# Kernel tuning notes

Hardware: AMD Instinct MI355X
Metric: run time of the kernel (lower is better)

The kernel has to match this reference:

```python
import jax, jax.numpy as jnp
import numpy as np
import math

FS = 44100.0
HOP = 256
N_BANDS = 24
KS_BUF = 768  # > max delay 44100/60 = 735 samples


def _lpc1(x, a):
    # order-1 all-pole (sample_wise_lpc with order 1, per-batch constant coeff):
    # y[n] = x[n] - a*y[n-1];  x: [B,N], a: [B]
    def step(yp, xt):
        y = xt - a * yp
        return y, y
    _, ys = jax.lax.scan(step, jnp.zeros_like(a), x.T)
    return ys.T


def _diff_ks(f0_frames, exc, l_b):
    # differentiable Karplus-Strong: fractional-delay loop + 2-tap damping filter.
    # f0_frames: [B,F] Hz, exc: [B,N], l_b: [B,F,2] (loop_coeff, loop_mix logits)
    B, N = exc.shape
    g = 0.999 * jax.nn.sigmoid(l_b[..., 0])   # loop gain in (0, 0.999)
    s = jax.nn.sigmoid(l_b[..., 1])           # loop-filter mix
    up = lambda p: jnp.repeat(p, HOP, axis=1)[:, :N]
    g_s, s_s = up(g), up(s)
    f0_s = up(jnp.clip(f0_frames, 60.0, None))
    D = jnp.clip(FS / f0_s, 2.0, 735.0)        # delay in samples
    Di = jnp.floor(D).astype(jnp.int32)
    fr = (D - Di).astype(exc.dtype)
    L = KS_BUF

    def step(carry, xs):
        buf, n = carry                         # buf: [B,L] circular delay line
        x_t, Di_t, fr_t, g_t, s_t = xs         # each [B]
        i1 = jnp.mod(n - Di_t, L)
        i2 = jnp.mod(n - Di_t - 1, L)
        i3 = jnp.mod(n - Di_t - 2, L)
        take = lambda i: jnp.take_along_axis(buf, i[:, None], axis=1)[:, 0]
        b1, b2, b3 = take(i1), take(i2), take(i3)
        z = (1.0 - fr_t) * b1 + fr_t * b2      # fractional-delay read y[n-D]
        z1 = (1.0 - fr_t) * b2 + fr_t * b3     # y[n-D-1]
        y = x_t + g_t * ((1.0 - s_t) * z + s_t * z1)
        buf = buf.at[:, jnp.mod(n, L)].set(y)
        return (buf, n + 1), y

    xs = (exc.T, Di.T, fr.T, g_s.T, s_s.T)
    init = (jnp.zeros((B, L), exc.dtype), jnp.int32(0))
    _, ys = jax.lax.scan(step, init, xs)
    return ys.T


def _body(x, body_gains):
    # bank of 24 two-pole resonators, log-spaced 80..8000 Hz, Q=10
    fc = jnp.geomspace(80.0, 8000.0, N_BANDS).astype(x.dtype)
    w = 2.0 * jnp.pi * fc / FS
    r = jnp.exp(-jnp.pi * fc / (10.0 * FS))
    a1 = -2.0 * r * jnp.cos(w)
    a2 = r * r
    b0 = 1.0 - r
    B = x.shape[0]

    def step(carry, xt):
        y1, y2 = carry                          # [B,24] each
        y = b0 * xt[:, None] - a1 * y1 - a2 * y2
        return (y, y1), jnp.sum(y * body_gains, axis=-1)

    init = (jnp.zeros((B, N_BANDS), x.dtype), jnp.zeros((B, N_BANDS), x.dtype))
    _, out = jax.lax.scan(step, init, x.T)
    return out.T


def _forward(excitation, pitch, w1, b1, w2, b2, excitation_gain, body_gains):
    B, _, N = excitation.shape
    h = jax.nn.relu(pitch @ w1.T + b1)
    mlp_out = h @ w2.T + b2                     # [B,3]
    loop_coeff = jnp.clip(mlp_out[:, 0], -2.0, 2.5)
    loop_mix = jnp.clip(mlp_out[:, 1], -2.5, 0.0)
    frames = N // HOP
    l_b = jnp.broadcast_to(jnp.stack([loop_coeff, loop_mix], -1)[:, None, :], (B, frames, 2))
    f0_frames = jnp.broadcast_to(pitch, (B, frames))
    exc_sq = (excitation * excitation_gain)[:, 0, :]
    f0_hz = jnp.clip(pitch[:, 0], 60.0, None)
    mult = jnp.clip(2.0 + 6.0 * (f0_hz - 60.0) / 600.0, 2.0, 8.0)
    cutoff = jnp.minimum(2.0 * jnp.pi * f0_hz * mult / FS, jnp.pi * 0.9)
    alpha = 1.0 - jnp.exp(-cutoff)
    exc_f = _lpc1(exc_sq * alpha[:, None], alpha - 1.0)   # pre-KS one-pole LP
    string = _diff_ks(f0_frames, exc_f, l_b)
    loop_post = jnp.clip(mlp_out[:, 2], -4.0, 4.0)
    cutoff_post = jnp.minimum(jnp.pi * jax.nn.sigmoid(loop_post), jnp.pi * 0.99)
    alpha_p = 1.0 - jnp.exp(-cutoff_post)
    string = _lpc1(string * alpha_p[:, None], alpha_p - 1.0)  # post one-pole LP
    out = _body(string, body_gains)
    return out[:, None, :], loop_coeff.mean(), loop_mix.mean(), loop_post.mean()


def setup_inputs():
    key = jax.random.key(0)
    k = jax.random.split(key, 6)
    B, N = 8, 32768
    excitation = jax.random.normal(k[0], (B, 1, N), dtype=jnp.float32)
    pitch = 60.0 + 600.0 * jax.random.uniform(k[1], (B, 1), dtype=jnp.float32)
    bnd1 = 0.1 * math.sqrt(6.0 / (1 + 16))   # xavier_uniform, gain 0.1
    bnd2 = 0.1 * math.sqrt(6.0 / (16 + 3))
    w1 = jax.random.uniform(k[2], (16, 1), jnp.float32, -bnd1, bnd1)
    b1 = jnp.zeros((16,), jnp.float32)
    w2 = jax.random.uniform(k[3], (3, 16), jnp.float32, -bnd2, bnd2)
    b2 = jnp.array([0.9, 0.0, 0.0], jnp.float32)
    excitation_gain = jnp.array(0.25, jnp.float32)
    body_gains = 0.006 * jnp.ones((1, N_BANDS), jnp.float32)
    return {"excitation": excitation, "pitch": pitch, "w1": w1, "b1": b1,
            "w2": w2, "b2": b2, "excitation_gain": excitation_gain,
            "body_gains": body_gains}


def reference(excitation, pitch, w1, b1, w2, b2, excitation_gain, body_gains):
    return _forward(excitation, pitch, w1, b1, w2, b2, excitation_gain, body_gains)
```

## Files before the change

kernel.cpp:

```cpp
#include <hip/hip_runtime.h>
#include <math.h>

#define NSAMP 32768
#define FS_F 44100.0f
#define PI_F 3.14159265358979323846f
#define T1 1024
#define FLAG_MAGIC 0x5A5A5A5A

#define XALL_FLOATS 33792
#define PROG_OFF 33792
#define TABS_OFF 33808
#define SMEM_FLOATS 40720

struct BParams {
  float alpha, alpha_p;
  float fr, g, s;
  int Di;
  float lc, lm, lp;
};

__device__ inline float sigmoidf_(float x) { return 1.0f / (1.0f + expf(-x)); }

__device__ inline BParams compute_params(int b, const float* __restrict__ pitch,
                                         const float* __restrict__ w1,
                                         const float* __restrict__ b1,
                                         const float* __restrict__ w2,
                                         const float* __restrict__ b2) {
  BParams P;
  float p = pitch[b];
  float h[16];
#pragma unroll
  for (int i = 0; i < 16; ++i) {
    float v = fmaf(p, w1[i], b1[i]);
    h[i] = v > 0.0f ? v : 0.0f;
  }
  float m[3];
#pragma unroll
  for (int j = 0; j < 3; ++j) {
    float acc = b2[j];
#pragma unroll
    for (int i = 0; i < 16; ++i) acc = fmaf(h[i], w2[j * 16 + i], acc);
    m[j] = acc;
  }
  P.lc = fminf(fmaxf(m[0], -2.0f), 2.5f);
  P.lm = fminf(fmaxf(m[1], -2.5f), 0.0f);
  P.lp = fminf(fmaxf(m[2], -4.0f), 4.0f);
  P.g = 0.999f * sigmoidf_(P.lc);
  P.s = sigmoidf_(P.lm);
  float f0 = fmaxf(p, 60.0f);
  float D = fminf(fmaxf(FS_F / f0, 2.0f), 735.0f);
  int Di = (int)floorf(D);
  P.fr = D - (float)Di;
  P.Di = Di;
  float mult = fminf(fmaxf(2.0f + 6.0f * (f0 - 60.0f) / 600.0f, 2.0f), 8.0f);
  float cutoff = fminf(2.0f * PI_F * f0 * mult / FS_F, PI_F * 0.9f);
  P.alpha = 1.0f - expf(-cutoff);
  float cpost = fminf(PI_F * sigmoidf_(P.lp), PI_F * 0.99f);
  P.alpha_p = 1.0f - expf(-cpost);
  return P;
}

__device__ inline float rlv(float v, int l) {
  return __int_as_float(__builtin_amdgcn_readlane(__float_as_int(v), l));
}
__device__ inline float shr1(float v, float bnd) {
  return __int_as_float(__builtin_amdgcn_update_dpp(
      __float_as_int(bnd), __float_as_int(v), 0x138 , 0xf, 0xf,
      false));
}
__device__ inline float ror1(float v) {
  return __int_as_float(__builtin_amdgcn_update_dpp(
      __float_as_int(v), __float_as_int(v), 0x13C , 0xf, 0xf,
      false));
}

__device__ inline void band_coef(int k, float& a1, float& a2, float& b0) {
  float fc = 80.0f * exp2f((float)k * (6.64385618977472436f / 23.0f));
  float w = 2.0f * PI_F * fc / FS_F;
  float r = expf(-PI_F * fc / (10.0f * FS_F));
  a1 = -2.0f * r * cosf(w);
  a2 = r * r;
  b0 = 1.0f - r;
}

__device__ inline void gen_tables(float* __restrict__ tabs, int W) {
  if (W >= 120) return;
  const int j = W / 5, sub = W % 5;
  float A1, A2, B0;
  band_coef(j, A1, A2, B0);
  if (sub == 0) *(float4*)&tabs[j * 4] = make_float4(A1, A2, B0, 0.f);
  float Q00 = -A1, Q01 = -A2, Q10 = 1.f, Q11 = 0.f;
#pragma unroll
  for (int sq = 0; sq < 2; ++sq) {
    float n00 = fmaf(Q00, Q00, Q01 * Q10);
    float n01 = fmaf(Q00, Q01, Q01 * Q11);
    float n10 = fmaf(Q10, Q00, Q11 * Q10);
    float n11 = fmaf(Q10, Q01, Q11 * Q11);
    Q00 = n00; Q01 = n01; Q10 = n10; Q11 = n11;
  }
  float K00 = Q00, K01 = Q01, K10 = Q10, K11 = Q11;
#pragma unroll
  for (int sq = 0; sq < 2; ++sq) {
    float n00 = fmaf(Q00, Q00, Q01 * Q10);
    float n01 = fmaf(Q00, Q01, Q01 * Q11);
    float n10 = fmaf(Q10, Q00, Q11 * Q10);
    float n11 = fmaf(Q10, Q01, Q11 * Q11);
    Q00 = n00; Q01 = n01; Q10 = n10; Q11 = n11;
  }
  float L00[7], L01[7], L10[7], L11[7];
  L00[0] = fmaf(Q00, K00, Q01 * K10);
  L01[0] = fmaf(Q00, K01, Q01 * K11);
  L10[0] = fmaf(Q10, K00, Q11 * K10);
  L11[0] = fmaf(Q10, K01, Q11 * K11);
#pragma unroll
  for (int k = 0; k < 6; ++k) {
    float s00 = fmaf(L00[k], L00[k], L01[k] * L10[k]);
    float s01 = fmaf(L00[k], L01[k], L01[k] * L11[k]);
    float s10 = fmaf(L10[k], L00[k], L11[k] * L10[k]);
    float s11 = fmaf(L10[k], L01[k], L11[k] * L11[k]);
    L00[k + 1] = s00; L01[k + 1] = s01; L10[k + 1] = s10; L11[k + 1] = s11;
  }
  if (sub == 0) {
#pragma unroll
    for (int k = 0; k < 6; ++k)
      *(float4*)&tabs[96 + (k * 24 + j) * 4] =
          make_float4(L00[k], L01[k], L10[k], L11[k]);
    *(float4*)&tabs[672 + j * 4] = make_float4(L00[6], L01[6], L10[6], L11[6]);
  }
  int l0 = sub * 13, l1 = l0 + 13;
  if (l1 > 64) l1 = 64;
  for (int l = l0; l < l1; ++l) {
    float R00 = 1.f, R01 = 0.f, R10 = 0.f, R11 = 1.f;
#pragma unroll
    for (int bit = 0; bit < 6; ++bit) {
      if ((l >> bit) & 1) {
        float n00 = fmaf(L00[bit], R00, L01[bit] * R10);
        float n01 = fmaf(L00[bit], R01, L01[bit] * R11);
        float n10 = fmaf(L10[bit], R00, L11[bit] * R10);
        float n11 = fmaf(L10[bit], R01, L11[bit] * R11);
        R00 = n00; R01 = n01; R10 = n10; R11 = n11;
      }
    }
    *(float4*)&tabs[768 + (j * 64 + l) * 4] = make_float4(R00, R01, R10, R11);
  }
}

__device__ inline void w1_load(const float* __restrict__ xg, int s1, int seg,
                               int lane, float4* pf) {
  const int base = s1 + (seg << 11) + (lane << 5);
#pragma unroll
  for (int i = 0; i < 8; ++i) {
    const int g = base + 4 * i;
    float4 v = make_float4(0.f, 0.f, 0.f, 0.f);
    if (g >= 0 && g + 3 < NSAMP) v = *(const float4*)&xg[g];
    pf[i] = v;
  }
}

#define KS_STEP(STORES)                                                       \
  do {                                                                        \
    float b2v[KNUM], b3v[KNUM];                                               \
    b2v[0] = shr1(yp[0], p1);                                                 \
    _Pragma("unroll") for (int k = 1; k < KNUM; ++k)                          \
        b2v[k] = shr1(yp[k], ror1(yp[k - 1]));                                \
    b3v[0] = shr1(b2v[0], p2);                                                \
    _Pragma("unroll") for (int k = 1; k < KNUM; ++k)                          \
        b3v[k] = shr1(b2v[k], ror1(b2v[k - 1]));                              \
    float p1n = rlv(yp[KNUM - 1], lq1);                                       \
    float p2n = rlv(b2v[KNUM - 1], lq1);                                      \
    _Pragma("unroll") for (int k = 0; k < KNUM; ++k)                          \
        yp[k] =                                                               \
            fmaf(c0w, yp[k], fmaf(c2w, b3v[k], fmaf(c1w, b2v[k], xC[k])));    \
    p1 = p1n;                                                                 \
    p2 = p2n;                                                                 \
    if (STORES) {                                                             \
      _Pragma("unroll") for (int k = 0; k < KNUM; ++k) {                      \
        int i = lane + (k << 6);                                              \
        int n = s1 + rel + i;                                                 \
        bool okl = (k < KNUM - 1) || (lane <= lq1);                           \
        if (okl && n >= n0 && n < end) yg[n] = yp[k];                         \
      }                                                                       \
    }                                                                         \
    int r2 = rel + 2 * C;                                                     \
    if (r2 < span) {                                                          \
      const float* xp = &xall[r2 + lane];                                     \
      _Pragma("unroll") for (int k = 0; k < KNUM; ++k) {                      \
        xC[k] = xN[k];                                                        \
        xN[k] = xp[k << 6];                                                   \
      }                                                                       \
    } else {                                                                  \
      _Pragma("unroll") for (int k = 0; k < KNUM; ++k) xC[k] = xN[k];         \
    }                                                                         \
    rel += C;                                                                 \
  } while (0)

template <int KNUM>
__device__ void ks_wave0(float* __restrict__ yg, const float* xall,
                         int* __restrict__ prog, int lane, int C, float c0w,
                         float c1w, float c2w, int s1, int n0, int end,
                         int span, int NSG) {
  const int lq1 = (C - 1) - (KNUM - 1) * 64;
  const int W = n0 - s1;
  float yp[KNUM], xC[KNUM], xN[KNUM];
  float p1 = 0.f, p2 = 0.f;
  int rel = 0;
#pragma unroll
  for (int k = 0; k < KNUM; ++k) { yp[k] = 0.f; xC[k] = 0.f; xN[k] = 0.f; }
  for (int s = 0; s < NSG; ++s) {
    int need = s + 3;
    if (need > NSG) need = NSG;
    while (__hip_atomic_load(prog, __ATOMIC_ACQUIRE,
                             __HIP_MEMORY_SCOPE_WORKGROUP) < need) {
      __builtin_amdgcn_s_sleep(1);
    }
    if (s == 0) {
#pragma unroll
      for (int k = 0; k < KNUM; ++k) {
        int i = lane + (k << 6);
        xC[k] = xall[i];
        xN[k] = xall[C + i];
      }
    }
    int fence = (s + 1) << 11;
    if (fence > span) fence = span;
    while (rel + 4 * C <= W && rel + 3 * C < fence) {
      KS_STEP(false); KS_STEP(false); KS_STEP(false); KS_STEP(false);
    }
    while (rel + C <= W && rel < fence) KS_STEP(false);
    while (rel + 3 * C < fence) {
      KS_STEP(true); KS_STEP(true); KS_STEP(true); KS_STEP(true);
    }
    while (rel < fence) KS_STEP(true);
  }
}

__device__ inline void ks_phase(int b, int q, const BParams& P,
                                const float* __restrict__ exc, float scale0,
                                float* __restrict__ buf1, float* xall,
                                int* prog, float* tabs, int t) {
  const int C = P.Di;
  const int n0 = q << 10;
  float lg = -logf(P.g);
  int Wp = (int)ceilf(10.5f / fmaxf(lg, 1e-6f));
  if (Wp > 64) Wp = 64;
  if (Wp < 4) Wp = 4;
  int W = Wp * C;
  if (W > n0) W = n0;
  W = (W + 3) & ~3;
  const int s1 = n0 - W;
  const int span = W + T1;
  const int end = n0 + T1;
  const int NSG = (span + 2047) >> 11;
  float* yg = buf1 + (size_t)b * NSAMP;
  const float* xg = exc + (size_t)b * NSAMP;

  const float c = 1.0f - P.alpha;
  const float scale = scale0 * P.alpha;
  const int lane = t & 63, wid = t >> 6;

  if (t == 0) *prog = 0;
  *(float4*)&xall[(NSG << 11) + 4 * t] = make_float4(0.f, 0.f, 0.f, 0.f);
  __syncthreads();

  const float c0w = P.g * (1.0f - P.s) * (1.0f - P.fr);
  const float c1w = P.g * ((1.0f - P.s) * P.fr + P.s * (1.0f - P.fr));
  const float c2w = P.g * P.s * P.fr;

  if (wid == 0) {
    switch ((C + 63) >> 6) {
      case 2:  ks_wave0<2>(yg, xall, prog, lane, C, c0w, c1w, c2w, s1, n0, end, span, NSG); break;
      case 3:  ks_wave0<3>(yg, xall, prog, lane, C, c0w, c1w, c2w, s1, n0, end, span, NSG); break;
      case 4:  ks_wave0<4>(yg, xall, prog, lane, C, c0w, c1w, c2w, s1, n0, end, span, NSG); break;
      case 5:  ks_wave0<5>(yg, xall, prog, lane, C, c0w, c1w, c2w, s1, n0, end, span, NSG); break;
      case 6:  ks_wave0<6>(yg, xall, prog, lane, C, c0w, c1w, c2w, s1, n0, end, span, NSG); break;
      case 7:  ks_wave0<7>(yg, xall, prog, lane, C, c0w, c1w, c2w, s1, n0, end, span, NSG); break;
      case 8:  ks_wave0<8>(yg, xall, prog, lane, C, c0w, c1w, c2w, s1, n0, end, span, NSG); break;
      case 9:  ks_wave0<9>(yg, xall, prog, lane, C, c0w, c1w, c2w, s1, n0, end, span, NSG); break;
      case 10: ks_wave0<10>(yg, xall, prog, lane, C, c0w, c1w, c2w, s1, n0, end, span, NSG); break;
      case 11: ks_wave0<11>(yg, xall, prog, lane, C, c0w, c1w, c2w, s1, n0, end, span, NSG); break;
      default: ks_wave0<12>(yg, xall, prog, lane, C, c0w, c1w, c2w, s1, n0, end, span, NSG); break;
    }
  } else if (wid == 1) {
    float c2v = c * c, c4 = c2v * c2v, c8 = c4 * c4;
    float m1 = c8, m2 = m1 * m1, m4 = m2 * m2, m8 = m4 * m4, m16 = m8 * m8,
          m32 = m16 * m16;
    float c512 = m32 * m32;
    float c1024 = c512 * c512;
    float c2048 = c1024 * c1024;
    const float n1 = m4, n2 = m8, n4 = m16, n8 = m32, n16 = c512,
                n32 = c512 * c512;
    const float c32lane = exp2f((float)(lane << 5) * log2f(c));
    float vrun = 0.0f;
    float4 pf[8], pg[8];
    w1_load(xg, s1, -1, lane, pf);
    w1_load(xg, s1, 0, lane, pg);
    for (int ls = -1; ls < NSG; ++ls) {
      float S = 0.0f;
#pragma unroll
      for (int i = 0; i < 8; ++i) {
        S = fmaf(c, S, scale * pf[i].x);
        S = fmaf(c, S, scale * pf[i].y);
        S = fmaf(c, S, scale * pf[i].z);
        S = fmaf(c, S, scale * pf[i].w);
      }
      float Sw = S, u;
      u = __shfl_up(Sw, 1);  if (lane >= 1)  Sw = fmaf(n1, u, Sw);
      u = __shfl_up(Sw, 2);  if (lane >= 2)  Sw = fmaf(n2, u, Sw);
      u = __shfl_up(Sw, 4);  if (lane >= 4)  Sw = fmaf(n4, u, Sw);
      u = __shfl_up(Sw, 8);  if (lane >= 8)  Sw = fmaf(n8, u, Sw);
      u = __shfl_up(Sw, 16); if (lane >= 16) Sw = fmaf(n16, u, Sw);
      u = __shfl_up(Sw, 32); if (lane >= 32) Sw = fmaf(n32, u, Sw);
      float tot = rlv(Sw, 63);
      float Sex = __shfl_up(Sw, 1);
      if (lane == 0) Sex = 0.0f;
      if (ls >= 0) {
        float v = fmaf(c32lane, vrun, Sex);
        const int o = (ls << 11) + (lane << 5);
#pragma unroll
        for (int i = 0; i < 8; ++i) {
          float4 y;
          v = fmaf(c, v, scale * pf[i].x); y.x = v;
          v = fmaf(c, v, scale * pf[i].y); y.y = v;
          v = fmaf(c, v, scale * pf[i].z); y.z = v;
          v = fmaf(c, v, scale * pf[i].w); y.w = v;
          *(float4*)&xall[o + 4 * i] = y;
        }
      }
      vrun = fmaf(c2048, vrun, tot);
      if (ls >= 0 && lane == 0) {
        __hip_atomic_store(prog, ls + 1, __ATOMIC_RELEASE,
                           __HIP_MEMORY_SCOPE_WORKGROUP);
      }
#pragma unroll
      for (int i = 0; i < 8; ++i) pf[i] = pg[i];
      if (ls + 2 < NSG) w1_load(xg, s1, ls + 2, lane, pg);
    }
  } else {
    gen_tables(tabs, (wid - 2) * 64 + lane);
  }
}

__device__ inline void lpc_lds(const float* __restrict__ xg,
                               float* __restrict__ sl, int s2, int nt, int lim,
                               float scale, float c, int t, float* lws) {
  const int lane = t & 63, wid = t >> 6;
  float c2v = c * c, c4 = c2v * c2v, c8 = c4 * c4;
  float m1 = c8, m2 = m1 * m1, m4 = m2 * m2, m8 = m4 * m4, m16 = m8 * m8,
        m32 = m16 * m16;
  float c512 = m32 * m32;
  float c2048 = c512 * c512;
  c2048 *= c2048;
  float l2c = log2f(c);
  float c8lane = exp2f((float)(8 * lane) * l2c);
  float cgk = exp2f((float)(8 * t) * l2c);
  float vrun = 0.0f;
  for (int tile = 0; tile < nt; ++tile) {
    __syncthreads();
    int g0 = s2 + (tile << 11) + 8 * t;
    float4 xa = make_float4(0.f, 0.f, 0.f, 0.f);
    float4 xb = make_float4(0.f, 0.f, 0.f, 0.f);
    if (g0 + 3 < lim) xa = *(const float4*)&xg[g0];
    if (g0 + 7 < lim) xb = *(const float4*)&xg[g0 + 4];
    float S = 0.0f;
    S = fmaf(c, S, scale * xa.x); S = fmaf(c, S, scale * xa.y);
    S = fmaf(c, S, scale * xa.z); S = fmaf(c, S, scale * xa.w);
    S = fmaf(c, S, scale * xb.x); S = fmaf(c, S, scale * xb.y);
    S = fmaf(c, S, scale * xb.z); S = fmaf(c, S, scale * xb.w);
    float Sw = S, u;
    u = __shfl_up(Sw, 1);  if (lane >= 1)  Sw = fmaf(m1, u, Sw);
    u = __shfl_up(Sw, 2);  if (lane >= 2)  Sw = fmaf(m2, u, Sw);
    u = __shfl_up(Sw, 4);  if (lane >= 4)  Sw = fmaf(m4, u, Sw);
    u = __shfl_up(Sw, 8);  if (lane >= 8)  Sw = fmaf(m8, u, Sw);
    u = __shfl_up(Sw, 16); if (lane >= 16) Sw = fmaf(m16, u, Sw);
    u = __shfl_up(Sw, 32); if (lane >= 32) Sw = fmaf(m32, u, Sw);
    if (lane == 63) lws[wid] = Sw;
    __syncthreads();
    float a0 = lws[0], a1w = lws[1], a2w = lws[2], a3w = lws[3];
    float carry = (wid == 1)   ? a0
                  : (wid == 2) ? fmaf(c512, a0, a1w)
                  : (wid == 3) ? fmaf(c512, fmaf(c512, a0, a1w), a2w)
                               : 0.0f;
    float Sprev = __shfl_up(Sw, 1);
    float Sex = (lane == 0) ? 0.0f : Sprev;
    Sex = fmaf(c8lane, carry, Sex);
    float v = fmaf(cgk, vrun, Sex);
    int o = g0 - s2;
    float4 ya, yb;
    v = fmaf(c, v, scale * xa.x); ya.x = v;
    v = fmaf(c, v, scale * xa.y); ya.y = v;
    v = fmaf(c, v, scale * xa.z); ya.z = v;
    v = fmaf(c, v, scale * xa.w); ya.w = v;
    v = fmaf(c, v, scale * xb.x); yb.x = v;
    v = fmaf(c, v, scale * xb.y); yb.y = v;
    v = fmaf(c, v, scale * xb.z); yb.z = v;
    v = fmaf(c, v, scale * xb.w); yb.w = v;
    *(float4*)&sl[o] = ya;
    *(float4*)&sl[o + 4] = yb;
    float tS = fmaf(c512, fmaf(c512, fmaf(c512, a0, a1w), a2w), a3w);
    vrun = fmaf(c2048, vrun, tS);
  }
}

__device__ inline void body_phase(int b, int q, const BParams& P,
                                  const float* __restrict__ gains,
                                  const float* __restrict__ buf1,
                                  float* __restrict__ out, float* sl,
                                  float* lws, float (*lc0)[8],
                                  float (*lc1)[8], const float* tabs, int t) {
  const int lane = t & 63, wid = t >> 6;
  const int n0 = q << 10;
  const int base = n0 - 4096;
  int s2 = base - 256;
  if (s2 < 0) s2 = 0;
  const int end = n0 + 1024;
  const int nt = (end - s2 + 2047) >> 11;

  lpc_lds(buf1 + (size_t)b * NSAMP, sl, s2, nt, end, P.alpha_p,
          1.0f - P.alpha_p, t, lws);
  __syncthreads();

  const float* bandcL = tabs;
  const float* QlevL = tabs + 96;
  const float* QwL = tabs + 672;
  const float* RtabL = tabs + 768;

  const int tb = base + 20 * t;
  float4 acc[5];
#pragma unroll
  for (int i = 0; i < 5; ++i) acc[i] = make_float4(0.f, 0.f, 0.f, 0.f);

  for (int g = 0; g < 3; ++g) {
    float A1[8], A2[8], B0[8], GN[8];
#pragma unroll
    for (int j = 0; j < 8; ++j) {
      int k = g * 8 + j;
      float4 bc = *(const float4*)&bandcL[k * 4];
      A1[j] = bc.x; A2[j] = bc.y; B0[j] = bc.z;
      GN[j] = gains[k];
    }
    float cv0[8], cv1[8];
#pragma unroll
    for (int j = 0; j < 8; ++j) cv0[j] = cv1[j] = 0.f;
    for (int i = 0; i < 5; ++i) {
      int n = tb + 4 * i;
      float4 xv = make_float4(0.f, 0.f, 0.f, 0.f);
      if (n >= 0) xv = *(const float4*)&sl[n - s2];
#pragma unroll
      for (int e = 0; e < 4; ++e) {
        float xi = e == 0 ? xv.x : e == 1 ? xv.y : e == 2 ? xv.z : xv.w;
#pragma unroll
        for (int j = 0; j < 8; ++j) {
          float nc = fmaf(B0[j], xi, -fmaf(A1[j], cv0[j], A2[j] * cv1[j]));
          cv1[j] = cv0[j];
          cv0[j] = nc;
        }
      }
    }
    int kl = 0;
    for (int off = 1; off <= 32; off <<= 1, ++kl) {
      float q00[8], q01[8], q10[8], q11[8];
#pragma unroll
      for (int j = 0; j < 8; ++j) {
        float4 qv = *(const float4*)&QlevL[(kl * 24 + g * 8 + j) * 4];
        q00[j] = qv.x; q01[j] = qv.y; q10[j] = qv.z; q11[j] = qv.w;
      }
#pragma unroll
      for (int j = 0; j < 8; ++j) {
        float u0 = __shfl_up(cv0[j], off);
        float u1 = __shfl_up(cv1[j], off);
        if (lane >= off) {
          float nc0 = fmaf(q00[j], u0, fmaf(q01[j], u1, cv0[j]));
          float nc1 = fmaf(q10[j], u0, fmaf(q11[j], u1, cv1[j]));
          cv0[j] = nc0;
          cv1[j] = nc1;
        }
      }
    }
    __syncthreads();
    if (lane == 63) {
#pragma unroll
      for (int j = 0; j < 8; ++j) {
        lc0[wid][j] = cv0[j];
        lc1[wid][j] = cv1[j];
      }
    }
    __syncthreads();
    float qw00[8], qw01[8], qw10[8], qw11[8];
#pragma unroll
    for (int j = 0; j < 8; ++j) {
      float4 qv = *(const float4*)&QwL[(g * 8 + j) * 4];
      qw00[j] = qv.x; qw01[j] = qv.y; qw10[j] = qv.z; qw11[j] = qv.w;
    }
    float car0[8], car1[8];
#pragma unroll
    for (int j = 0; j < 8; ++j) car0[j] = car1[j] = 0.f;
    for (int v = 0; v < wid; ++v) {
#pragma unroll
      for (int j = 0; j < 8; ++j) {
        float n0c = fmaf(qw00[j], car0[j], fmaf(qw01[j], car1[j], lc0[v][j]));
        float n1c = fmaf(qw10[j], car0[j], fmaf(qw11[j], car1[j], lc1[v][j]));
        car0[j] = n0c;
        car1[j] = n1c;
      }
    }
    float y1[8], y2[8];
#pragma unroll
    for (int j = 0; j < 8; ++j) {
      float4 rv = *(const float4*)&RtabL[((g * 8 + j) * 64 + lane) * 4];
      float e0 = __shfl_up(cv0[j], 1);
      float e1 = __shfl_up(cv1[j], 1);
      if (lane == 0) { e0 = 0.f; e1 = 0.f; }
      y1[j] = fmaf(rv.x, car0[j], fmaf(rv.y, car1[j], e0));
      y2[j] = fmaf(rv.z, car0[j], fmaf(rv.w, car1[j], e1));
    }
    if (tb + 20 > n0) {
      for (int i = 0; i < 5; ++i) {
        float4 xv = *(const float4*)&sl[tb - s2 + 4 * i];
        float4 ov = acc[i];
#pragma unroll
        for (int e = 0; e < 4; ++e) {
          float xi = e == 0 ? xv.x : e == 1 ? xv.y : e == 2 ? xv.z : xv.w;
          float a = 0.f;
#pragma unroll
          for (int j = 0; j < 8; ++j) {
            float yv = fmaf(B0[j], xi, -fmaf(A1[j], y1[j], A2[j] * y2[j]));
            y2[j] = y1[j];
            y1[j] = yv;
            a = fmaf(GN[j], yv, a);
          }
          if (e == 0) ov.x += a;
          else if (e == 1) ov.y += a;
          else if (e == 2) ov.z += a;
          else ov.w += a;
        }
        acc[i] = ov;
      }
    }
  }
  if (tb + 20 > n0) {
    float* outb = out + (size_t)b * NSAMP;
#pragma unroll
    for (int i = 0; i < 5; ++i) {
      int n = tb + 4 * i;
      if (n >= n0) *(float4*)&outb[n] = acc[i];
    }
  }
}

__global__ void __launch_bounds__(256, 1) synth_all(
    const float* __restrict__ exc, const float* __restrict__ pitch,
    const float* __restrict__ w1, const float* __restrict__ b1,
    const float* __restrict__ w2, const float* __restrict__ b2,
    const float* __restrict__ eg, const float* __restrict__ gains,
    float* __restrict__ buf1, int* __restrict__ flags,
    float* __restrict__ out) {
  extern __shared__ float smem[];
  const int blk = blockIdx.x;
  const int b = blk >> 5, q = blk & 31;
  const int t = threadIdx.x;

  BParams P = compute_params(b, pitch, w1, b1, w2, b2);
  if (blk == 0 && t < 64) {
    int bb = (t < 8) ? t : 0;
    BParams Q = compute_params(bb, pitch, w1, b1, w2, b2);
    float slc = 0.f, slm = 0.f, slp = 0.f;
    for (int i = 0; i < 8; ++i) {
      slc += rlv(Q.lc, i);
      slm += rlv(Q.lm, i);
      slp += rlv(Q.lp, i);
    }
    if (t == 0) {
      out[8 * NSAMP + 0] = slc / 8.0f;
      out[8 * NSAMP + 1] = slm / 8.0f;
      out[8 * NSAMP + 2] = slp / 8.0f;
    }
  }

  ks_phase(b, q, P, exc, eg[0], buf1, smem, (int*)&smem[PROG_OFF],
           smem + TABS_OFF, t);
  __syncthreads();

  const int n0 = q << 10;
  int s2 = n0 - 4096 - 256;
  if (s2 < 0) s2 = 0;
  const int qlo = s2 >> 10;
  if (t == 0) {
    __hip_atomic_store(&flags[blk], FLAG_MAGIC, __ATOMIC_RELEASE,
                       __HIP_MEMORY_SCOPE_AGENT);
    for (int f = qlo; f < q; ++f) {
      while (__hip_atomic_load(&flags[b * 32 + f], __ATOMIC_ACQUIRE,
                               __HIP_MEMORY_SCOPE_AGENT) != FLAG_MAGIC) {
        __builtin_amdgcn_s_sleep(8);
      }
    }
  }
  __syncthreads();

  body_phase(b, q, P, gains, buf1, out, smem, smem + 6144,
             (float(*)[8])(smem + 6152), (float(*)[8])(smem + 6184),
             smem + TABS_OFF, t);
}

extern "C" void kernel_launch(void* const* d_in, const int* in_sizes, int n_in,
                              void* d_out, int out_size, void* d_ws, size_t ws_size,
                              hipStream_t stream) {
  const float* exc = (const float*)d_in[0];
  const float* pitch = (const float*)d_in[1];
  const float* w1 = (const float*)d_in[2];
  const float* b1 = (const float*)d_in[3];
  const float* w2 = (const float*)d_in[4];
  const float* b2 = (const float*)d_in[5];
  const float* eg = (const float*)d_in[6];
  const float* bg = (const float*)d_in[7];
  float* out = (float*)d_out;
  float* buf1 = (float*)d_ws;
  int* flags = (int*)(buf1 + 8 * NSAMP);

  static int lds_set = 0;
  if (!lds_set) {
    hipFuncSetAttribute(reinterpret_cast<const void*>(synth_all),
                        hipFuncAttributeMaxDynamicSharedMemorySize,
                        SMEM_FLOATS * 4);
    lds_set = 1;
  }
  hipLaunchKernelGGL(synth_all, dim3(256), dim3(256), SMEM_FLOATS * 4, stream,
                     exc, pitch, w1, b1, w2, b2, eg, bg, buf1, flags, out);
}
```

Baseline: 115.0 us.

## Parallelize excitation LPC prefill across three waves with per-segment ready flags

The order-1 LPC prefill of the excitation, previously run serially by one wave with a running carry, is now split across waves 1-3 in round-robin segments. Each segment rebuilds its carry-in from a truncated recurrence over the previous 2048-sample segment. A single progress counter becomes per-segment flags that the KS wave polls one by one. The 4x unrolled KS step loops are also removed, and table generation moves onto waves 1-2 after their LPC work. The truncated carry is an approximation that relies on c^2048 being negligible, and each segment now does redundant work on the preceding block.

```diff
diff --git a/kernel.cpp b/kernel.cpp
--- a/kernel.cpp
+++ b/kernel.cpp
@@ -204,14 +204,17 @@
   float yp[KNUM], xC[KNUM], xN[KNUM];
   float p1 = 0.f, p2 = 0.f;
   int rel = 0;
+  int done = 0;
 #pragma unroll
   for (int k = 0; k < KNUM; ++k) { yp[k] = 0.f; xC[k] = 0.f; xN[k] = 0.f; }
   for (int s = 0; s < NSG; ++s) {
     int need = s + 3;
     if (need > NSG) need = NSG;
-    while (__hip_atomic_load(prog, __ATOMIC_ACQUIRE,
-                             __HIP_MEMORY_SCOPE_WORKGROUP) < need) {
-      __builtin_amdgcn_s_sleep(1);
+    for (; done < need; ++done) {
+      while (__hip_atomic_load(&prog[done], __ATOMIC_ACQUIRE,
+                               __HIP_MEMORY_SCOPE_WORKGROUP) == 0) {
+        __builtin_amdgcn_s_sleep(1);
+      }
     }
     if (s == 0) {
 #pragma unroll
@@ -223,13 +226,7 @@
     }
     int fence = (s + 1) << 11;
     if (fence > span) fence = span;
-    while (rel + 4 * C <= W && rel + 3 * C < fence) {
-      KS_STEP(false); KS_STEP(false); KS_STEP(false); KS_STEP(false);
-    }
     while (rel + C <= W && rel < fence) KS_STEP(false);
-    while (rel + 3 * C < fence) {
-      KS_STEP(true); KS_STEP(true); KS_STEP(true); KS_STEP(true);
-    }
     while (rel < fence) KS_STEP(true);
   }
 }
@@ -258,7 +255,7 @@
   const float scale = scale0 * P.alpha;
   const int lane = t & 63, wid = t >> 6;
 
-  if (t == 0) *prog = 0;
+  if (t < 16) prog[t] = 0;
   *(float4*)&xall[(NSG << 11) + 4 * t] = make_float4(0.f, 0.f, 0.f, 0.f);
   __syncthreads();
 
@@ -280,21 +277,34 @@
       case 11: ks_wave0<11>(yg, xall, prog, lane, C, c0w, c1w, c2w, s1, n0, end, span, NSG); break;
       default: ks_wave0<12>(yg, xall, prog, lane, C, c0w, c1w, c2w, s1, n0, end, span, NSG); break;
     }
-  } else if (wid == 1) {
+  } else {
     float c2v = c * c, c4 = c2v * c2v, c8 = c4 * c4;
     float m1 = c8, m2 = m1 * m1, m4 = m2 * m2, m8 = m4 * m4, m16 = m8 * m8,
           m32 = m16 * m16;
     float c512 = m32 * m32;
-    float c1024 = c512 * c512;
-    float c2048 = c1024 * c1024;
     const float n1 = m4, n2 = m8, n4 = m16, n8 = m32, n16 = c512,
                 n32 = c512 * c512;
     const float c32lane = exp2f((float)(lane << 5) * log2f(c));
-    float vrun = 0.0f;
-    float4 pf[8], pg[8];
-    w1_load(xg, s1, -1, lane, pf);
-    w1_load(xg, s1, 0, lane, pg);
-    for (int ls = -1; ls < NSG; ++ls) {
+    for (int ls = wid - 1; ls < NSG; ls += 3) {
+      float4 pp[8], pf[8];
+      w1_load(xg, s1, ls - 1, lane, pp);
+      w1_load(xg, s1, ls, lane, pf);
+      float Sp = 0.0f;
+#pragma unroll
+      for (int i = 0; i < 8; ++i) {
+        Sp = fmaf(c, Sp, scale * pp[i].x);
+        Sp = fmaf(c, Sp, scale * pp[i].y);
+        Sp = fmaf(c, Sp, scale * pp[i].z);
+        Sp = fmaf(c, Sp, scale * pp[i].w);
+      }
+      float Swp = Sp, up;
+      up = __shfl_up(Swp, 1);  if (lane >= 1)  Swp = fmaf(n1, up, Swp);
+      up = __shfl_up(Swp, 2);  if (lane >= 2)  Swp = fmaf(n2, up, Swp);
+      up = __shfl_up(Swp, 4);  if (lane >= 4)  Swp = fmaf(n4, up, Swp);
+      up = __shfl_up(Swp, 8);  if (lane >= 8)  Swp = fmaf(n8, up, Swp);
+      up = __shfl_up(Swp, 16); if (lane >= 16) Swp = fmaf(n16, up, Swp);
+      up = __shfl_up(Swp, 32); if (lane >= 32) Swp = fmaf(n32, up, Swp);
+      float tpre = rlv(Swp, 63);
       float S = 0.0f;
 #pragma unroll
       for (int i = 0; i < 8; ++i) {
@@ -310,33 +320,25 @@
       u = __shfl_up(Sw, 8);  if (lane >= 8)  Sw = fmaf(n8, u, Sw);
       u = __shfl_up(Sw, 16); if (lane >= 16) Sw = fmaf(n16, u, Sw);
       u = __shfl_up(Sw, 32); if (lane >= 32) Sw = fmaf(n32, u, Sw);
-      float tot = rlv(Sw, 63);
       float Sex = __shfl_up(Sw, 1);
       if (lane == 0) Sex = 0.0f;
-      if (ls >= 0) {
-        float v = fmaf(c32lane, vrun, Sex);
-        const int o = (ls << 11) + (lane << 5);
-#pragma unroll
-        for (int i = 0; i < 8; ++i) {
-          float4 y;
-          v = fmaf(c, v, scale * pf[i].x); y.x = v;
-          v = fmaf(c, v, scale * pf[i].y); y.y = v;
-          v = fmaf(c, v, scale * pf[i].z); y.z = v;
-          v = fmaf(c, v, scale * pf[i].w); y.w = v;
-          *(float4*)&xall[o + 4 * i] = y;
-        }
-      }
-      vrun = fmaf(c2048, vrun, tot);
-      if (ls >= 0 && lane == 0) {
-        __hip_atomic_store(prog, ls + 1, __ATOMIC_RELEASE,
+      float v = fmaf(c32lane, tpre, Sex);
+      const int o = (ls << 11) + (lane << 5);
+#pragma unroll
+      for (int i = 0; i < 8; ++i) {
+        float4 y;
+        v = fmaf(c, v, scale * pf[i].x); y.x = v;
+        v = fmaf(c, v, scale * pf[i].y); y.y = v;
+        v = fmaf(c, v, scale * pf[i].z); y.z = v;
+        v = fmaf(c, v, scale * pf[i].w); y.w = v;
+        *(float4*)&xall[o + 4 * i] = y;
+      }
+      if (lane == 0) {
+        __hip_atomic_store(&prog[ls], 1, __ATOMIC_RELEASE,
                            __HIP_MEMORY_SCOPE_WORKGROUP);
       }
-#pragma unroll
-      for (int i = 0; i < 8; ++i) pf[i] = pg[i];
-      if (ls + 2 < NSG) w1_load(xg, s1, ls + 2, lane, pg);
-    }
-  } else {
-    gen_tables(tabs, (wid - 2) * 64 + lane);
+    }
+    if (wid <= 2) gen_tables(tabs, (wid - 1) * 64 + lane);
   }
 }
 
@@ -618,9 +620,9 @@
 
   static int lds_set = 0;
   if (!lds_set) {
-    hipFuncSetAttribute(reinterpret_cast<const void*>(synth_all),
-                        hipFuncAttributeMaxDynamicSharedMemorySize,
-                        SMEM_FLOATS * 4);
+    (void)hipFuncSetAttribute(reinterpret_cast<const void*>(synth_all),
+                              hipFuncAttributeMaxDynamicSharedMemorySize,
+                              SMEM_FLOATS * 4);
     lds_set = 1;
   }
   hipLaunchKernelGGL(synth_all, dim3(256), dim3(256), SMEM_FLOATS * 4, stream,
```

Result: faster. 111.4 us (-3.1%).
